# Kernel tuning notes

Hardware: AMD Instinct MI355X
Metric: run time of the kernel (lower is better)

## Reference

```python
import jax, jax.numpy as jnp
import numpy as np
from jax.ops import segment_sum

N_NODES = 100000
N_EDGES = 1600000
N_GRAPHS = 128
HIDDEN = 128
N_CLASSES = 10


def setup_inputs() -> dict:
    key = jax.random.key(0)
    ks = jax.random.split(key, 8)
    src = jax.random.randint(ks[0], (N_EDGES,), 0, N_NODES, dtype=jnp.int32)
    dst = jax.random.randint(ks[1], (N_EDGES,), 0, N_NODES, dtype=jnp.int32)
    graph_ids = jnp.sort(jax.random.randint(ks[2], (N_NODES,), 0, N_GRAPHS, dtype=jnp.int32))
    W1 = jax.random.normal(ks[3], (1, HIDDEN), dtype=jnp.float32)
    b1 = jnp.zeros((HIDDEN,), jnp.float32)
    W2 = jax.random.normal(ks[4], (HIDDEN, HIDDEN), dtype=jnp.float32) * 0.05
    b2 = jnp.zeros((HIDDEN,), jnp.float32)
    Wc = jax.random.normal(ks[5], (HIDDEN, N_CLASSES), dtype=jnp.float32) * 0.05
    bc = jnp.zeros((N_CLASSES,), jnp.float32)
    return {"src": src, "dst": dst, "graph_ids": graph_ids,
            "W1": W1, "b1": b1, "W2": W2, "b2": b2, "Wc": Wc, "bc": bc}


def _graph_conv(h, src, dst, norm_src, norm_dst, W, b, n_nodes):
    # DGL GraphConv, norm='both': D_out^{-1/2} gather -> scatter-sum -> W -> D_in^{-1/2} -> +b
    hs = h * norm_src[:, None]
    agg = segment_sum(hs[src], dst, num_segments=n_nodes)  # [N, F_in]
    return agg @ W * norm_dst[:, None] + b


def reference(src, dst, graph_ids, W1, b1, W2, b2, Wc, bc):
    n_nodes = graph_ids.shape[0]
    ones_e = jnp.ones(src.shape[0], jnp.float32)
    indeg = segment_sum(ones_e, dst, num_segments=n_nodes)
    outdeg = segment_sum(ones_e, src, num_segments=n_nodes)
    norm_src = jnp.clip(outdeg, 1.0, None) ** -0.5
    norm_dst = jnp.clip(indeg, 1.0, None) ** -0.5

    h = indeg[:, None]  # node feature = in-degree, [N, 1]
    h = jax.nn.relu(_graph_conv(h, src, dst, norm_src, norm_dst, W1, b1, n_nodes))
    h = jax.nn.relu(_graph_conv(h, src, dst, norm_src, norm_dst, W2, b2, n_nodes))

    # dgl.mean_nodes: per-graph mean pooling
    sums = segment_sum(h, graph_ids, num_segments=N_GRAPHS)          # [G, H]
    cnts = segment_sum(jnp.ones(n_nodes, jnp.float32), graph_ids, num_segments=N_GRAPHS)
    hg = sums / jnp.clip(cnts, 1.0, None)[:, None]
    return hg @ Wc + bc  # [G, n_classes]
```

## Files before the change

kernel.cpp:

```cpp
#include <hip/hip_runtime.h>

#define N_NODES   100000
#define N_EDGES   1600000
#define N_GRAPHS  128
#define HIDDEN    128
#define N_CLASSES 10

#define BSH   9
#define BSZ   512
#define NBUCK 196
#define CAP   16384
#define PCH   4096
#define PTH   512
#define PIT   (PCH / PTH)

typedef unsigned int   uint;
typedef unsigned short ushort;
typedef unsigned char  uchar;

__global__ __launch_bounds__(PTH)
void k_part(const int* __restrict__ src, const int* __restrict__ dst,
            unsigned* __restrict__ bcur1, unsigned* __restrict__ bcur2,
            unsigned* __restrict__ tmp1, ushort* __restrict__ tmp2, int nE) {
    __shared__ unsigned hist[256], scanT[256], lcur[256], base[256];
    __shared__ unsigned stag4[PCH];
    __shared__ uchar    stagB[PCH];
    int t = threadIdx.x;
    int e0 = blockIdx.x * PCH;
    int e1 = min(e0 + PCH, nE);
    int cntE = e1 - e0;

    int sv[PIT], dv[PIT];
    if (t < 256) hist[t] = 0;
    __syncthreads();
    #pragma unroll
    for (int m = 0; m < PIT; ++m) {
        int e = e0 + t + m * PTH;
        if (e < e1) {
            sv[m] = src[e]; dv[m] = dst[e];
            atomicAdd(&hist[dv[m] >> BSH], 1u);
        }
    }
    __syncthreads();
    unsigned v = (t < 256) ? hist[t] : 0u;
    if (t < 256) scanT[t] = v;
    __syncthreads();
    for (int off = 1; off < 256; off <<= 1) {
        unsigned add = (t < 256 && t >= off) ? scanT[t - off] : 0u;
        __syncthreads();
        if (t < 256) scanT[t] += add;
        __syncthreads();
    }
    if (t < 256) {
        unsigned excl = scanT[t] - v;
        lcur[t] = excl;
        if (v > 0) { unsigned g = atomicAdd(&bcur1[t], v); base[t] = (unsigned)t * CAP + g - excl; }
    }
    __syncthreads();
    #pragma unroll
    for (int m = 0; m < PIT; ++m) {
        int e = e0 + t + m * PTH;
        if (e < e1) {
            int d = dv[m], s = sv[m];
            int b = d >> BSH;
            unsigned p = atomicAdd(&lcur[b], 1u);
            stag4[p] = ((unsigned)(d & (BSZ - 1)) << 17) | (unsigned)s;
            stagB[p] = (uchar)b;
        }
    }
    __syncthreads();
    for (int i = t; i < cntE; i += PTH) {
        unsigned b = stagB[i];
        unsigned a = base[b] + (unsigned)i;
        if (a < (b + 1u) * CAP) tmp1[a] = stag4[i];
    }
    __syncthreads();

    if (t < 256) hist[t] = 0;
    __syncthreads();
    #pragma unroll
    for (int m = 0; m < PIT; ++m) {
        int e = e0 + t + m * PTH;
        if (e < e1) atomicAdd(&hist[sv[m] >> BSH], 1u);
    }
    __syncthreads();
    v = (t < 256) ? hist[t] : 0u;
    if (t < 256) scanT[t] = v;
    __syncthreads();
    for (int off = 1; off < 256; off <<= 1) {
        unsigned add = (t < 256 && t >= off) ? scanT[t - off] : 0u;
        __syncthreads();
        if (t < 256) scanT[t] += add;
        __syncthreads();
    }
    if (t < 256) {
        unsigned excl = scanT[t] - v;
        lcur[t] = excl;
        if (v > 0) { unsigned g = atomicAdd(&bcur2[t], v); base[t] = (unsigned)t * CAP + g - excl; }
    }
    __syncthreads();
    #pragma unroll
    for (int m = 0; m < PIT; ++m) {
        int e = e0 + t + m * PTH;
        if (e < e1) {
            int s = sv[m];
            unsigned p = atomicAdd(&lcur[s >> BSH], 1u);
            stag4[p] = (unsigned)s;
        }
    }
    __syncthreads();
    for (int i = t; i < cntE; i += PTH) {
        unsigned s = stag4[i];
        unsigned b = s >> BSH;
        unsigned a = base[b] + (unsigned)i;
        if (a < (b + 1u) * CAP) tmp2[a] = (ushort)(s & (BSZ - 1));
    }
}

__global__ __launch_bounds__(1024)
void k_ind_csr(const unsigned* __restrict__ bcur1, const unsigned* __restrict__ tmp1,
               const unsigned* __restrict__ bcur2, const ushort* __restrict__ tmp2,
               unsigned* __restrict__ rsind, float* __restrict__ ns,
               float* __restrict__ hs0, int* __restrict__ csr) {
    __shared__ unsigned cin[BSZ], cout[BSZ], pref[BSZ], lcur[BSZ];
    int b = blockIdx.x, t = threadIdx.x;
    if (t < BSZ) { cin[t] = 0; cout[t] = 0; }
    __syncthreads();
    unsigned f1 = min(bcur1[b], (unsigned)CAP);
    const unsigned* tp1 = tmp1 + (size_t)b * CAP;
    for (unsigned i = t; i < f1; i += 1024) atomicAdd(&cin[tp1[i] >> 17], 1u);
    unsigned f2 = min(bcur2[b], (unsigned)CAP);
    const ushort* tp2 = tmp2 + (size_t)b * CAP;
    for (unsigned i = t; i < f2; i += 1024) atomicAdd(&cout[tp2[i]], 1u);
    __syncthreads();
    unsigned v = (t < BSZ) ? cin[t] : 0u;
    if (t < BSZ) pref[t] = v;
    __syncthreads();
    for (int off = 1; off < BSZ; off <<= 1) {
        unsigned add = (t < BSZ && t >= off) ? pref[t - off] : 0u;
        __syncthreads();
        if (t < BSZ) pref[t] += add;
        __syncthreads();
    }
    if (t < BSZ) {
        unsigned excl = pref[t] - v;
        lcur[t] = excl;
        int n = b * BSZ + t;
        if (n < N_NODES) {
            unsigned co = cout[t];
            float nsv = rsqrtf(fmaxf((float)co, 1.0f));
            ns[n]    = nsv;
            hs0[n]   = (float)v * nsv;
            rsind[n] = (((unsigned)b * CAP + excl) << 10) | min(v, 1023u);
        }
    }
    __syncthreads();
    int* cb = csr + (size_t)b * CAP;
    for (unsigned i = t; i < f1; i += 1024) {
        unsigned e = tp1[i];
        unsigned pos = atomicAdd(&lcur[e >> 17], 1u);
        cb[pos] = (int)(e & 0x1FFFFu);
    }
}

__global__ __launch_bounds__(256)
void k_conv1_info(const unsigned* __restrict__ rsind, const int* __restrict__ csr,
                  const float* __restrict__ hs0, const float* __restrict__ ns,
                  const float* __restrict__ W1, const float* __restrict__ b1,
                  const float* __restrict__ W2,
                  float* __restrict__ U, float* __restrict__ V,
                  float4* __restrict__ info, int nN) {
    __shared__ float stu[128];
    __shared__ float sts[128];
    int t = threadIdx.x;
    if (t < 128) {
        float w = W1[t], bb = b1[t];
        stu[t] = (w != 0.0f) ? (-bb / w) : 1e30f;
    }
    __syncthreads();
    if (blockIdx.x < 129) {
        if (t < 128) sts[t] = stu[t];
        __syncthreads();
        for (int k = 2; k <= 128; k <<= 1) {
            for (int j = k >> 1; j > 0; j >>= 1) {
                if (t < 128) {
                    int ixj = t ^ j;
                    if (ixj > t) {
                        float a = sts[t], bb = sts[ixj];
                        bool up = ((t & k) == 0);
                        if (up ? (a > bb) : (a < bb)) { sts[t] = bb; sts[ixj] = a; }
                    }
                }
                __syncthreads();
            }
        }
        if (t < 128) {
            int sg = blockIdx.x;
            float a_rep;
            if (sg == 0)        a_rep = sts[0]   - 1.0f;
            else if (sg == 128) a_rep = sts[127] + 1.0f;
            else                a_rep = 0.5f * (sts[sg - 1] + sts[sg]);
            float u = 0.0f, vv = 0.0f;
            #pragma unroll 8
            for (int j = 0; j < 128; ++j) {
                float w  = W1[j], bb = b1[j];
                float w2 = W2[j * HIDDEN + t];
                bool on  = (a_rep * w + bb > 0.0f);
                u  += on ? w  * w2 : 0.0f;
                vv += on ? bb * w2 : 0.0f;
            }
            U[sg * HIDDEN + t] = u;
            V[sg * HIDDEN + t] = vv;
        }
    }
    int node = blockIdx.x * 128 + (t >> 1);
    if (node >= nN) return;
    int j  = t & 1;
    unsigned rix = rsind[node];
    int r0 = (int)(rix >> 10);
    int c  = (int)(rix & 1023u);
    float a = 0.0f;
    #pragma unroll 4
    for (int k = j; k < c; k += 2) a += hs0[csr[r0 + k]];
    a += __shfl_xor(a, 1);
    float nd = rsqrtf(fmaxf((float)c, 1.0f));
    float av = a * nd;
    int sgp = 0;
    #pragma unroll
    for (int q = 0; q < 64; ++q) sgp += (stu[j * 64 + q] < av) ? 1 : 0;
    sgp += __shfl_xor(sgp, 1);
    if (j == 0) {
        float nsv = ns[node];
        info[node] = make_float4(nsv * av, nsv, __int_as_float(sgp), nd);
    }
}

__global__ __launch_bounds__(256)
void k_conv2_pool(const unsigned* __restrict__ rsind, const int* __restrict__ csr,
                  const float4* __restrict__ info,
                  const float* __restrict__ U, const float* __restrict__ V,
                  const int* __restrict__ graph_ids, const float* __restrict__ b2,
                  float* __restrict__ pool, float* __restrict__ cnt, int nN) {
    __shared__ float sA[64], sB[64], sND[64];
    __shared__ int   sSg[64], sGr[64], sR[64], sC[64];
    __shared__ float sRes[64][HIDDEN];
    int blockBase = blockIdx.x * 64;
    int t = threadIdx.x;
    int node = blockBase + (t >> 2);
    int j = t & 3;

    float A = 0.0f, B = 0.0f;
    int mn = 255, mx = 0;
    int r0 = 0, c = 0;
    if (node < nN) {
        unsigned rix = rsind[node];
        r0 = (int)(rix >> 10); c = (int)(rix & 1023u);
        #pragma unroll 4
        for (int k = j; k < c; k += 4) {
            float4 nf = info[csr[r0 + k]];
            int sg = __float_as_int(nf.z);
            A += nf.x; B += nf.y;
            mn = min(mn, sg); mx = max(mx, sg);
        }
    }
    A += __shfl_xor(A, 1); A += __shfl_xor(A, 2);
    B += __shfl_xor(B, 1); B += __shfl_xor(B, 2);
    mn = min(mn, __shfl_xor(mn, 1)); mn = min(mn, __shfl_xor(mn, 2));
    mx = max(mx, __shfl_xor(mx, 1)); mx = max(mx, __shfl_xor(mx, 2));
    if (node < nN && j == 0) {
        int i = t >> 2;
        sA[i] = A; sB[i] = B;
        sSg[i] = (mn << 8) | mx;
        sR[i] = r0; sC[i] = c;
        sND[i] = info[node].w;
        sGr[i] = graph_ids[node];
    }
    __syncthreads();

    int w = t >> 6, lane = t & 63;
    float bb0 = b2[lane], bb1 = b2[64 + lane];
    for (int i = w * 16; i < w * 16 + 16; ++i) {
        int n = blockBase + i;
        if (n >= nN) break;
        int pk = sSg[i], smn = pk >> 8, smx = pk & 255;
        float acc0, acc1;
        if (smn >= smx) {
            int sg = min(smn, 128);
            float Av = sA[i], Bv = sB[i];
            const float* Ur = U + sg * HIDDEN;
            const float* Vr = V + sg * HIDDEN;
            acc0 = Av * Ur[lane]      + Bv * Vr[lane];
            acc1 = Av * Ur[64 + lane] + Bv * Vr[64 + lane];
        } else {
            acc0 = 0.0f; acc1 = 0.0f;
            int rr = sR[i], cc = sC[i];
            for (int k = 0; k < cc; ++k) {
                float4 nf = info[csr[rr + k]];
                int sg = __float_as_int(nf.z);
                const float* Ur = U + sg * HIDDEN;
                const float* Vr = V + sg * HIDDEN;
                acc0 += nf.x * Ur[lane]      + nf.y * Vr[lane];
                acc1 += nf.x * Ur[64 + lane] + nf.y * Vr[64 + lane];
            }
        }
        float nd = sND[i];
        sRes[i][lane]      = fmaxf(nd * acc0 + bb0, 0.0f);
        sRes[i][64 + lane] = fmaxf(nd * acc1 + bb1, 0.0f);
    }
    __syncthreads();

    if (t >= 64) return;
    int lane0 = t;
    int gcur = -1;
    float racc0 = 0.0f, racc1 = 0.0f, cl = 0.0f;
    for (int i = 0; i < 64; ++i) {
        int n = blockBase + i;
        if (n >= nN) break;
        float r0v = sRes[i][lane0];
        float r1v = sRes[i][64 + lane0];
        int g = sGr[i];
        if (g != gcur) {
            if (gcur >= 0) {
                atomicAdd(&pool[gcur * HIDDEN + lane0],      racc0);
                atomicAdd(&pool[gcur * HIDDEN + 64 + lane0], racc1);
                if (lane0 == 0) atomicAdd(&cnt[gcur], cl);
            }
            gcur = g; racc0 = 0.0f; racc1 = 0.0f; cl = 0.0f;
        }
        racc0 += r0v; racc1 += r1v; cl += 1.0f;
    }
    if (gcur >= 0) {
        atomicAdd(&pool[gcur * HIDDEN + lane0],      racc0);
        atomicAdd(&pool[gcur * HIDDEN + 64 + lane0], racc1);
        if (lane0 == 0) atomicAdd(&cnt[gcur], cl);
    }
}

__global__ void k_final(const float* __restrict__ pool, const float* __restrict__ cnt,
                        const float* __restrict__ Wc, const float* __restrict__ bc,
                        float* __restrict__ out) {
    int t = blockIdx.x * blockDim.x + threadIdx.x;
    if (t >= N_GRAPHS * N_CLASSES) return;
    int g = t / N_CLASSES, c = t % N_CLASSES;
    float inv = 1.0f / fmaxf(cnt[g], 1.0f);
    float acc = bc[c];
    for (int j = 0; j < HIDDEN; ++j)
        acc += pool[g * HIDDEN + j] * inv * Wc[j * N_CLASSES + c];
    out[t] = acc;
}

extern "C" void kernel_launch(void* const* d_in, const int* in_sizes, int n_in,
                              void* d_out, int out_size, void* d_ws, size_t ws_size,
                              hipStream_t stream) {
    const int*   src       = (const int*)d_in[0];
    const int*   dst       = (const int*)d_in[1];
    const int*   graph_ids = (const int*)d_in[2];
    const float* W1        = (const float*)d_in[3];
    const float* b1        = (const float*)d_in[4];
    const float* W2        = (const float*)d_in[5];
    const float* b2        = (const float*)d_in[6];
    const float* Wc        = (const float*)d_in[7];
    const float* bc        = (const float*)d_in[8];
    float* out = (float*)d_out;

    char* ws = (char*)d_ws;
    size_t off = 0;
    auto alloc = [&](size_t elems) { void* p = ws + off; off += elems * 4; return p; };

    unsigned* bcur1 = (unsigned*)alloc(256);
    unsigned* bcur2 = (unsigned*)alloc(256);
    float*    pool  = (float*)   alloc(N_GRAPHS * HIDDEN);
    float*    cnt   = (float*)   alloc(N_GRAPHS);
    size_t zero_bytes = off;
    float4*   info  = (float4*)  alloc((size_t)N_NODES * 4);
    unsigned* tmp1  = (unsigned*)alloc((size_t)NBUCK * CAP);
    ushort*   tmp2  = (ushort*)  alloc((size_t)NBUCK * CAP / 2);
    int*      csr   = (int*)     alloc((size_t)NBUCK * CAP);
    unsigned* rsind = (unsigned*)alloc(N_NODES);
    float*    nsA   = (float*)   alloc(N_NODES);
    float*    hs0   = (float*)   alloc(N_NODES);
    float*    U     = (float*)   alloc(129 * HIDDEN);
    float*    V     = (float*)   alloc(129 * HIDDEN);

    hipMemsetAsync(d_ws, 0, zero_bytes, stream);

    int pblocks  = (N_EDGES + PCH - 1) / PCH;
    int c1blocks = (N_NODES + 127) / 128;
    int c2blocks = (N_NODES + 63) / 64;
    k_part      <<<pblocks, PTH, 0, stream>>>(src, dst, bcur1, bcur2, tmp1, tmp2, N_EDGES);
    k_ind_csr   <<<NBUCK, 1024, 0, stream>>>(bcur1, tmp1, bcur2, tmp2, rsind, nsA, hs0, csr);
    k_conv1_info<<<c1blocks, 256, 0, stream>>>(rsind, csr, hs0, nsA, W1, b1, W2, U, V, info, N_NODES);
    k_conv2_pool<<<c2blocks, 256, 0, stream>>>(rsind, csr, info, U, V, graph_ids, b2, pool, cnt, N_NODES);
    k_final     <<<(N_GRAPHS * N_CLASSES + 255) / 256, 256, 0, stream>>>(pool, cnt, Wc, bc, out);
}
```

Before: 169.1 us.

## Replace bucketed CSR partitioning with global atomic degree count, scan and fill

The two-stage bucket partition (LDS histograms, staging buffers, per-bucket CSR build) is replaced by three simpler passes. k_deg counts in- and out-degree with global atomics, k_scan does a block-wise prefix scan using an atomic block base, and k_fill places edges into the CSR with atomic cursors. k_fill also accumulates the first-layer aggregation with float atomics, so conv1 no longer needs a separate CSR gather. The aim is to cut the partition overhead and one full edge traversal. The cost is millions of random global atomics, a nondeterministic CSR order and a nondeterministic float summation order.

```diff
diff --git a/kernel.cpp b/kernel.cpp
--- a/kernel.cpp
+++ b/kernel.cpp
@@ -6,170 +6,77 @@
 #define HIDDEN    128
 #define N_CLASSES 10
 
-#define BSH   9
-#define BSZ   512
-#define NBUCK 196
-#define CAP   16384
-#define PCH   4096
-#define PTH   512
-#define PIT   (PCH / PTH)
-
 typedef unsigned int   uint;
 typedef unsigned short ushort;
-typedef unsigned char  uchar;
-
-__global__ __launch_bounds__(PTH)
-void k_part(const int* __restrict__ src, const int* __restrict__ dst,
-            unsigned* __restrict__ bcur1, unsigned* __restrict__ bcur2,
-            unsigned* __restrict__ tmp1, ushort* __restrict__ tmp2, int nE) {
-    __shared__ unsigned hist[256], scanT[256], lcur[256], base[256];
-    __shared__ unsigned stag4[PCH];
-    __shared__ uchar    stagB[PCH];
+
+__global__ __launch_bounds__(256)
+void k_deg(const int4* __restrict__ src4, const int4* __restrict__ dst4,
+           uint* __restrict__ indeg, uint* __restrict__ outdeg, int nE4) {
+    int i = blockIdx.x * 256 + threadIdx.x;
+    if (i >= nE4) return;
+    int4 s = src4[i], d = dst4[i];
+    atomicAdd(&outdeg[s.x], 1u); atomicAdd(&outdeg[s.y], 1u);
+    atomicAdd(&outdeg[s.z], 1u); atomicAdd(&outdeg[s.w], 1u);
+    atomicAdd(&indeg[d.x], 1u);  atomicAdd(&indeg[d.y], 1u);
+    atomicAdd(&indeg[d.z], 1u);  atomicAdd(&indeg[d.w], 1u);
+}
+
+__global__ __launch_bounds__(1024)
+void k_scan(const uint* __restrict__ indeg, const uint* __restrict__ outdeg,
+            uint* __restrict__ etotal, uint* __restrict__ cur,
+            uint* __restrict__ rsind, float* __restrict__ ns,
+            float* __restrict__ hs0, int nN) {
+    __shared__ uint sc[1024];
+    __shared__ uint sbase;
     int t = threadIdx.x;
-    int e0 = blockIdx.x * PCH;
-    int e1 = min(e0 + PCH, nE);
-    int cntE = e1 - e0;
-
-    int sv[PIT], dv[PIT];
-    if (t < 256) hist[t] = 0;
-    __syncthreads();
-    #pragma unroll
-    for (int m = 0; m < PIT; ++m) {
-        int e = e0 + t + m * PTH;
-        if (e < e1) {
-            sv[m] = src[e]; dv[m] = dst[e];
-            atomicAdd(&hist[dv[m] >> BSH], 1u);
-        }
-    }
-    __syncthreads();
-    unsigned v = (t < 256) ? hist[t] : 0u;
-    if (t < 256) scanT[t] = v;
-    __syncthreads();
-    for (int off = 1; off < 256; off <<= 1) {
-        unsigned add = (t < 256 && t >= off) ? scanT[t - off] : 0u;
+    int n = blockIdx.x * 1024 + t;
+    uint v = (n < nN) ? indeg[n] : 0u;
+    sc[t] = v;
+    __syncthreads();
+    for (int off = 1; off < 1024; off <<= 1) {
+        uint add = (t >= off) ? sc[t - off] : 0u;
         __syncthreads();
-        if (t < 256) scanT[t] += add;
+        sc[t] += add;
         __syncthreads();
     }
-    if (t < 256) {
-        unsigned excl = scanT[t] - v;
-        lcur[t] = excl;
-        if (v > 0) { unsigned g = atomicAdd(&bcur1[t], v); base[t] = (unsigned)t * CAP + g - excl; }
-    }
-    __syncthreads();
-    #pragma unroll
-    for (int m = 0; m < PIT; ++m) {
-        int e = e0 + t + m * PTH;
-        if (e < e1) {
-            int d = dv[m], s = sv[m];
-            int b = d >> BSH;
-            unsigned p = atomicAdd(&lcur[b], 1u);
-            stag4[p] = ((unsigned)(d & (BSZ - 1)) << 17) | (unsigned)s;
-            stagB[p] = (uchar)b;
-        }
-    }
-    __syncthreads();
-    for (int i = t; i < cntE; i += PTH) {
-        unsigned b = stagB[i];
-        unsigned a = base[b] + (unsigned)i;
-        if (a < (b + 1u) * CAP) tmp1[a] = stag4[i];
-    }
-    __syncthreads();
-
-    if (t < 256) hist[t] = 0;
-    __syncthreads();
-    #pragma unroll
-    for (int m = 0; m < PIT; ++m) {
-        int e = e0 + t + m * PTH;
-        if (e < e1) atomicAdd(&hist[sv[m] >> BSH], 1u);
-    }
-    __syncthreads();
-    v = (t < 256) ? hist[t] : 0u;
-    if (t < 256) scanT[t] = v;
-    __syncthreads();
-    for (int off = 1; off < 256; off <<= 1) {
-        unsigned add = (t < 256 && t >= off) ? scanT[t - off] : 0u;
-        __syncthreads();
-        if (t < 256) scanT[t] += add;
-        __syncthreads();
-    }
-    if (t < 256) {
-        unsigned excl = scanT[t] - v;
-        lcur[t] = excl;
-        if (v > 0) { unsigned g = atomicAdd(&bcur2[t], v); base[t] = (unsigned)t * CAP + g - excl; }
-    }
-    __syncthreads();
-    #pragma unroll
-    for (int m = 0; m < PIT; ++m) {
-        int e = e0 + t + m * PTH;
-        if (e < e1) {
-            int s = sv[m];
-            unsigned p = atomicAdd(&lcur[s >> BSH], 1u);
-            stag4[p] = (unsigned)s;
-        }
-    }
-    __syncthreads();
-    for (int i = t; i < cntE; i += PTH) {
-        unsigned s = stag4[i];
-        unsigned b = s >> BSH;
-        unsigned a = base[b] + (unsigned)i;
-        if (a < (b + 1u) * CAP) tmp2[a] = (ushort)(s & (BSZ - 1));
-    }
-}
-
-__global__ __launch_bounds__(1024)
-void k_ind_csr(const unsigned* __restrict__ bcur1, const unsigned* __restrict__ tmp1,
-               const unsigned* __restrict__ bcur2, const ushort* __restrict__ tmp2,
-               unsigned* __restrict__ rsind, float* __restrict__ ns,
-               float* __restrict__ hs0, int* __restrict__ csr) {
-    __shared__ unsigned cin[BSZ], cout[BSZ], pref[BSZ], lcur[BSZ];
-    int b = blockIdx.x, t = threadIdx.x;
-    if (t < BSZ) { cin[t] = 0; cout[t] = 0; }
-    __syncthreads();
-    unsigned f1 = min(bcur1[b], (unsigned)CAP);
-    const unsigned* tp1 = tmp1 + (size_t)b * CAP;
-    for (unsigned i = t; i < f1; i += 1024) atomicAdd(&cin[tp1[i] >> 17], 1u);
-    unsigned f2 = min(bcur2[b], (unsigned)CAP);
-    const ushort* tp2 = tmp2 + (size_t)b * CAP;
-    for (unsigned i = t; i < f2; i += 1024) atomicAdd(&cout[tp2[i]], 1u);
-    __syncthreads();
-    unsigned v = (t < BSZ) ? cin[t] : 0u;
-    if (t < BSZ) pref[t] = v;
-    __syncthreads();
-    for (int off = 1; off < BSZ; off <<= 1) {
-        unsigned add = (t < BSZ && t >= off) ? pref[t - off] : 0u;
-        __syncthreads();
-        if (t < BSZ) pref[t] += add;
-        __syncthreads();
-    }
-    if (t < BSZ) {
-        unsigned excl = pref[t] - v;
-        lcur[t] = excl;
-        int n = b * BSZ + t;
-        if (n < N_NODES) {
-            unsigned co = cout[t];
-            float nsv = rsqrtf(fmaxf((float)co, 1.0f));
-            ns[n]    = nsv;
-            hs0[n]   = (float)v * nsv;
-            rsind[n] = (((unsigned)b * CAP + excl) << 10) | min(v, 1023u);
-        }
-    }
-    __syncthreads();
-    int* cb = csr + (size_t)b * CAP;
-    for (unsigned i = t; i < f1; i += 1024) {
-        unsigned e = tp1[i];
-        unsigned pos = atomicAdd(&lcur[e >> 17], 1u);
-        cb[pos] = (int)(e & 0x1FFFFu);
+    if (t == 1023) sbase = atomicAdd(etotal, sc[1023]);
+    __syncthreads();
+    if (n < nN) {
+        uint incl = sc[t];
+        uint row  = sbase + incl - v;
+        uint od   = outdeg[n];
+        float nsv = rsqrtf(fmaxf((float)od, 1.0f));
+        ns[n]    = nsv;
+        hs0[n]   = (float)v * nsv;
+        cur[n]   = row;
+        rsind[n] = (row << 10) | min(v, 1023u);
     }
 }
 
 __global__ __launch_bounds__(256)
-void k_conv1_info(const unsigned* __restrict__ rsind, const int* __restrict__ csr,
-                  const float* __restrict__ hs0, const float* __restrict__ ns,
-                  const float* __restrict__ W1, const float* __restrict__ b1,
-                  const float* __restrict__ W2,
-                  float* __restrict__ U, float* __restrict__ V,
-                  float4* __restrict__ info, int nN) {
+void k_fill(const int4* __restrict__ src4, const int4* __restrict__ dst4,
+            const float* __restrict__ hs0, uint* __restrict__ cur,
+            int* __restrict__ csr, float* __restrict__ agg1, int nE4) {
+    int i = blockIdx.x * 256 + threadIdx.x;
+    if (i >= nE4) return;
+    int4 s = src4[i], d = dst4[i];
+    float h0 = hs0[s.x], h1 = hs0[s.y], h2 = hs0[s.z], h3 = hs0[s.w];
+    uint p0 = atomicAdd(&cur[d.x], 1u);
+    uint p1 = atomicAdd(&cur[d.y], 1u);
+    uint p2 = atomicAdd(&cur[d.z], 1u);
+    uint p3 = atomicAdd(&cur[d.w], 1u);
+    csr[p0] = s.x; csr[p1] = s.y; csr[p2] = s.z; csr[p3] = s.w;
+    atomicAdd(&agg1[d.x], h0); atomicAdd(&agg1[d.y], h1);
+    atomicAdd(&agg1[d.z], h2); atomicAdd(&agg1[d.w], h3);
+}
+
+__global__ __launch_bounds__(256)
+void k_info(const uint* __restrict__ indeg, const float* __restrict__ agg1,
+            const float* __restrict__ ns,
+            const float* __restrict__ W1, const float* __restrict__ b1,
+            const float* __restrict__ W2,
+            float* __restrict__ U, float* __restrict__ V,
+            float4* __restrict__ info, int nN) {
     __shared__ float stu[128];
     __shared__ float sts[128];
     int t = threadIdx.x;
@@ -213,30 +120,20 @@
             V[sg * HIDDEN + t] = vv;
         }
     }
-    int node = blockIdx.x * 128 + (t >> 1);
+    int node = blockIdx.x * 256 + t;
     if (node >= nN) return;
-    int j  = t & 1;
-    unsigned rix = rsind[node];
-    int r0 = (int)(rix >> 10);
-    int c  = (int)(rix & 1023u);
-    float a = 0.0f;
-    #pragma unroll 4
-    for (int k = j; k < c; k += 2) a += hs0[csr[r0 + k]];
-    a += __shfl_xor(a, 1);
+    uint c   = indeg[node];
     float nd = rsqrtf(fmaxf((float)c, 1.0f));
-    float av = a * nd;
+    float av = agg1[node] * nd;
     int sgp = 0;
-    #pragma unroll
-    for (int q = 0; q < 64; ++q) sgp += (stu[j * 64 + q] < av) ? 1 : 0;
-    sgp += __shfl_xor(sgp, 1);
-    if (j == 0) {
-        float nsv = ns[node];
-        info[node] = make_float4(nsv * av, nsv, __int_as_float(sgp), nd);
-    }
+    #pragma unroll 16
+    for (int q = 0; q < 128; ++q) sgp += (stu[q] < av) ? 1 : 0;
+    float nsv = ns[node];
+    info[node] = make_float4(nsv * av, nsv, __int_as_float(sgp), nd);
 }
 
 __global__ __launch_bounds__(256)
-void k_conv2_pool(const unsigned* __restrict__ rsind, const int* __restrict__ csr,
+void k_conv2_pool(const uint* __restrict__ rsind, const int* __restrict__ csr,
                   const float4* __restrict__ info,
                   const float* __restrict__ U, const float* __restrict__ V,
                   const int* __restrict__ graph_ids, const float* __restrict__ b2,
@@ -253,7 +150,7 @@
     int mn = 255, mx = 0;
     int r0 = 0, c = 0;
     if (node < nN) {
-        unsigned rix = rsind[node];
+        uint rix = rsind[node];
         r0 = (int)(rix >> 10); c = (int)(rix & 1023u);
         #pragma unroll 4
         for (int k = j; k < c; k += 4) {
@@ -367,29 +264,39 @@
     size_t off = 0;
     auto alloc = [&](size_t elems) { void* p = ws + off; off += elems * 4; return p; };
 
-    unsigned* bcur1 = (unsigned*)alloc(256);
-    unsigned* bcur2 = (unsigned*)alloc(256);
-    float*    pool  = (float*)   alloc(N_GRAPHS * HIDDEN);
-    float*    cnt   = (float*)   alloc(N_GRAPHS);
+    uint*  indeg  = (uint*) alloc(N_NODES);
+    uint*  outdeg = (uint*) alloc(N_NODES);
+    float* agg1   = (float*)alloc(N_NODES);
+    float* pool   = (float*)alloc(N_GRAPHS * HIDDEN);
+    float* cnt    = (float*)alloc(N_GRAPHS);
+    uint*  etotal = (uint*) alloc(4);
     size_t zero_bytes = off;
-    float4*   info  = (float4*)  alloc((size_t)N_NODES * 4);
-    unsigned* tmp1  = (unsigned*)alloc((size_t)NBUCK * CAP);
-    ushort*   tmp2  = (ushort*)  alloc((size_t)NBUCK * CAP / 2);
-    int*      csr   = (int*)     alloc((size_t)NBUCK * CAP);
-    unsigned* rsind = (unsigned*)alloc(N_NODES);
-    float*    nsA   = (float*)   alloc(N_NODES);
-    float*    hs0   = (float*)   alloc(N_NODES);
-    float*    U     = (float*)   alloc(129 * HIDDEN);
-    float*    V     = (float*)   alloc(129 * HIDDEN);
+    uint*   cur   = (uint*)  alloc(N_NODES);
+    uint*   rsind = (uint*)  alloc(N_NODES);
+    float*  nsA   = (float*) alloc(N_NODES);
+    float*  hs0   = (float*) alloc(N_NODES);
+    float4* info  = (float4*)alloc((size_t)N_NODES * 4);
+    int*    csr   = (int*)   alloc((size_t)N_EDGES);
+    float*  U     = (float*) alloc(129 * HIDDEN);
+    float*  V     = (float*) alloc(129 * HIDDEN);
 
     hipMemsetAsync(d_ws, 0, zero_bytes, stream);
 
-    int pblocks  = (N_EDGES + PCH - 1) / PCH;
-    int c1blocks = (N_NODES + 127) / 128;
+    int nE4      = N_EDGES / 4;
+    int eblocks  = (nE4 + 255) / 256;
+    int sblocks  = (N_NODES + 1023) / 1024;
+    int iblocks  = (N_NODES + 255) / 256;
     int c2blocks = (N_NODES + 63) / 64;
-    k_part      <<<pblocks, PTH, 0, stream>>>(src, dst, bcur1, bcur2, tmp1, tmp2, N_EDGES);
-    k_ind_csr   <<<NBUCK, 1024, 0, stream>>>(bcur1, tmp1, bcur2, tmp2, rsind, nsA, hs0, csr);
-    k_conv1_info<<<c1blocks, 256, 0, stream>>>(rsind, csr, hs0, nsA, W1, b1, W2, U, V, info, N_NODES);
-    k_conv2_pool<<<c2blocks, 256, 0, stream>>>(rsind, csr, info, U, V, graph_ids, b2, pool, cnt, N_NODES);
+
+    k_deg       <<<eblocks, 256, 0, stream>>>((const int4*)src, (const int4*)dst,
+                                              indeg, outdeg, nE4);
+    k_scan      <<<sblocks, 1024, 0, stream>>>(indeg, outdeg, etotal, cur,
+                                               rsind, nsA, hs0, N_NODES);
+    k_fill      <<<eblocks, 256, 0, stream>>>((const int4*)src, (const int4*)dst,
+                                              hs0, cur, csr, agg1, nE4);
+    k_info      <<<iblocks, 256, 0, stream>>>(indeg, agg1, nsA, W1, b1, W2,
+                                              U, V, info, N_NODES);
+    k_conv2_pool<<<c2blocks, 256, 0, stream>>>(rsind, csr, info, U, V,
+                                               graph_ids, b2, pool, cnt, N_NODES);
     k_final     <<<(N_GRAPHS * N_CLASSES + 255) / 256, 256, 0, stream>>>(pool, cnt, Wc, bc, out);
 }
```

New measurement: 412.4 us. 144% more time.

## Drop CSR build; aggregate per-bucket edges via shared-memory atomics

Applied to the files above, without the earlier changes.

Removes the per-bucket prefix scan and CSR scatter. Both convolution stages now work directly on the bucketed edge list, with one block per 512-node bucket accumulating into shared memory through atomics. The mixed-segment fallback rescans the whole bucket edge list for each node that needs it. Only 196 blocks are launched, so the GPU is underutilised, and the fallback path can be very expensive.

```diff
diff --git a/kernel.cpp b/kernel.cpp
--- a/kernel.cpp
+++ b/kernel.cpp
@@ -118,11 +118,10 @@
 }
 
 __global__ __launch_bounds__(1024)
-void k_ind_csr(const unsigned* __restrict__ bcur1, const unsigned* __restrict__ tmp1,
-               const unsigned* __restrict__ bcur2, const ushort* __restrict__ tmp2,
-               unsigned* __restrict__ rsind, float* __restrict__ ns,
-               float* __restrict__ hs0, int* __restrict__ csr) {
-    __shared__ unsigned cin[BSZ], cout[BSZ], pref[BSZ], lcur[BSZ];
+void k_cnt(const unsigned* __restrict__ bcur1, const unsigned* __restrict__ tmp1,
+           const unsigned* __restrict__ bcur2, const ushort* __restrict__ tmp2,
+           float* __restrict__ ns, float* __restrict__ hs0, float* __restrict__ ndv) {
+    __shared__ unsigned cin[BSZ], cout[BSZ];
     int b = blockIdx.x, t = threadIdx.x;
     if (t < BSZ) { cin[t] = 0; cout[t] = 0; }
     __syncthreads();
@@ -133,52 +132,37 @@
     const ushort* tp2 = tmp2 + (size_t)b * CAP;
     for (unsigned i = t; i < f2; i += 1024) atomicAdd(&cout[tp2[i]], 1u);
     __syncthreads();
-    unsigned v = (t < BSZ) ? cin[t] : 0u;
-    if (t < BSZ) pref[t] = v;
-    __syncthreads();
-    for (int off = 1; off < BSZ; off <<= 1) {
-        unsigned add = (t < BSZ && t >= off) ? pref[t - off] : 0u;
-        __syncthreads();
-        if (t < BSZ) pref[t] += add;
-        __syncthreads();
-    }
     if (t < BSZ) {
-        unsigned excl = pref[t] - v;
-        lcur[t] = excl;
         int n = b * BSZ + t;
         if (n < N_NODES) {
-            unsigned co = cout[t];
-            float nsv = rsqrtf(fmaxf((float)co, 1.0f));
-            ns[n]    = nsv;
-            hs0[n]   = (float)v * nsv;
-            rsind[n] = (((unsigned)b * CAP + excl) << 10) | min(v, 1023u);
-        }
-    }
-    __syncthreads();
-    int* cb = csr + (size_t)b * CAP;
-    for (unsigned i = t; i < f1; i += 1024) {
-        unsigned e = tp1[i];
-        unsigned pos = atomicAdd(&lcur[e >> 17], 1u);
-        cb[pos] = (int)(e & 0x1FFFFu);
-    }
-}
-
-__global__ __launch_bounds__(256)
-void k_conv1_info(const unsigned* __restrict__ rsind, const int* __restrict__ csr,
-                  const float* __restrict__ hs0, const float* __restrict__ ns,
-                  const float* __restrict__ W1, const float* __restrict__ b1,
-                  const float* __restrict__ W2,
-                  float* __restrict__ U, float* __restrict__ V,
-                  float4* __restrict__ info, int nN) {
+            unsigned ci = cin[t];
+            float nsv = rsqrtf(fmaxf((float)cout[t], 1.0f));
+            ns[n]  = nsv;
+            hs0[n] = (float)ci * nsv;
+            ndv[n] = rsqrtf(fmaxf((float)ci, 1.0f));
+        }
+    }
+}
+
+__global__ __launch_bounds__(512)
+void k_info(const unsigned* __restrict__ bcur1, const unsigned* __restrict__ tmp1,
+            const float* __restrict__ hs0, const float* __restrict__ ns,
+            const float* __restrict__ ndv,
+            const float* __restrict__ W1, const float* __restrict__ b1,
+            const float* __restrict__ W2,
+            float* __restrict__ U, float* __restrict__ V,
+            float4* __restrict__ info) {
+    __shared__ float agg[BSZ];
     __shared__ float stu[128];
     __shared__ float sts[128];
-    int t = threadIdx.x;
+    int b = blockIdx.x, t = threadIdx.x;
+    agg[t] = 0.0f;
     if (t < 128) {
         float w = W1[t], bb = b1[t];
         stu[t] = (w != 0.0f) ? (-bb / w) : 1e30f;
     }
     __syncthreads();
-    if (blockIdx.x < 129) {
+    if (b < 129) {
         if (t < 128) sts[t] = stu[t];
         __syncthreads();
         for (int k = 2; k <= 128; k <<= 1) {
@@ -195,7 +179,7 @@
             }
         }
         if (t < 128) {
-            int sg = blockIdx.x;
+            int sg = b;
             float a_rep;
             if (sg == 0)        a_rep = sts[0]   - 1.0f;
             else if (sg == 128) a_rep = sts[127] + 1.0f;
@@ -213,126 +197,88 @@
             V[sg * HIDDEN + t] = vv;
         }
     }
-    int node = blockIdx.x * 128 + (t >> 1);
-    if (node >= nN) return;
-    int j  = t & 1;
-    unsigned rix = rsind[node];
-    int r0 = (int)(rix >> 10);
-    int c  = (int)(rix & 1023u);
-    float a = 0.0f;
-    #pragma unroll 4
-    for (int k = j; k < c; k += 2) a += hs0[csr[r0 + k]];
-    a += __shfl_xor(a, 1);
-    float nd = rsqrtf(fmaxf((float)c, 1.0f));
-    float av = a * nd;
-    int sgp = 0;
-    #pragma unroll
-    for (int q = 0; q < 64; ++q) sgp += (stu[j * 64 + q] < av) ? 1 : 0;
-    sgp += __shfl_xor(sgp, 1);
-    if (j == 0) {
-        float nsv = ns[node];
-        info[node] = make_float4(nsv * av, nsv, __int_as_float(sgp), nd);
-    }
-}
-
-__global__ __launch_bounds__(256)
-void k_conv2_pool(const unsigned* __restrict__ rsind, const int* __restrict__ csr,
-                  const float4* __restrict__ info,
-                  const float* __restrict__ U, const float* __restrict__ V,
-                  const int* __restrict__ graph_ids, const float* __restrict__ b2,
-                  float* __restrict__ pool, float* __restrict__ cnt, int nN) {
-    __shared__ float sA[64], sB[64], sND[64];
-    __shared__ int   sSg[64], sGr[64], sR[64], sC[64];
-    __shared__ float sRes[64][HIDDEN];
-    int blockBase = blockIdx.x * 64;
-    int t = threadIdx.x;
-    int node = blockBase + (t >> 2);
-    int j = t & 3;
-
-    float A = 0.0f, B = 0.0f;
-    int mn = 255, mx = 0;
-    int r0 = 0, c = 0;
-    if (node < nN) {
-        unsigned rix = rsind[node];
-        r0 = (int)(rix >> 10); c = (int)(rix & 1023u);
-        #pragma unroll 4
-        for (int k = j; k < c; k += 4) {
-            float4 nf = info[csr[r0 + k]];
-            int sg = __float_as_int(nf.z);
-            A += nf.x; B += nf.y;
-            mn = min(mn, sg); mx = max(mx, sg);
-        }
-    }
-    A += __shfl_xor(A, 1); A += __shfl_xor(A, 2);
-    B += __shfl_xor(B, 1); B += __shfl_xor(B, 2);
-    mn = min(mn, __shfl_xor(mn, 1)); mn = min(mn, __shfl_xor(mn, 2));
-    mx = max(mx, __shfl_xor(mx, 1)); mx = max(mx, __shfl_xor(mx, 2));
-    if (node < nN && j == 0) {
-        int i = t >> 2;
-        sA[i] = A; sB[i] = B;
-        sSg[i] = (mn << 8) | mx;
-        sR[i] = r0; sC[i] = c;
-        sND[i] = info[node].w;
-        sGr[i] = graph_ids[node];
-    }
-    __syncthreads();
-
-    int w = t >> 6, lane = t & 63;
-    float bb0 = b2[lane], bb1 = b2[64 + lane];
-    for (int i = w * 16; i < w * 16 + 16; ++i) {
-        int n = blockBase + i;
-        if (n >= nN) break;
-        int pk = sSg[i], smn = pk >> 8, smx = pk & 255;
-        float acc0, acc1;
-        if (smn >= smx) {
-            int sg = min(smn, 128);
-            float Av = sA[i], Bv = sB[i];
-            const float* Ur = U + sg * HIDDEN;
-            const float* Vr = V + sg * HIDDEN;
-            acc0 = Av * Ur[lane]      + Bv * Vr[lane];
-            acc1 = Av * Ur[64 + lane] + Bv * Vr[64 + lane];
+    unsigned f1 = min(bcur1[b], (unsigned)CAP);
+    const unsigned* tp1 = tmp1 + (size_t)b * CAP;
+    for (unsigned i = t; i < f1; i += 512) {
+        unsigned e = tp1[i];
+        atomicAdd(&agg[e >> 17], hs0[e & 0x1FFFFu]);
+    }
+    __syncthreads();
+    int n = b * BSZ + t;
+    if (n < N_NODES) {
+        float nd = ndv[n];
+        float av = agg[t] * nd;
+        int sgp = 0;
+        #pragma unroll 16
+        for (int q = 0; q < 128; ++q) sgp += (stu[q] < av) ? 1 : 0;
+        float nsv = ns[n];
+        info[n] = make_float4(nsv * av, nsv, __int_as_float(sgp), nd);
+    }
+}
+
+__global__ __launch_bounds__(512)
+void k_conv2(const unsigned* __restrict__ bcur1, const unsigned* __restrict__ tmp1,
+             const float4* __restrict__ info,
+             const float* __restrict__ U, const float* __restrict__ V,
+             const int* __restrict__ graph_ids, const float* __restrict__ b2,
+             float* __restrict__ pool, float* __restrict__ cnt) {
+    __shared__ float aggA[BSZ], aggB[BSZ];
+    __shared__ uint  smn[BSZ], smx[BSZ];
+    int b = blockIdx.x, t = threadIdx.x;
+    aggA[t] = 0.0f; aggB[t] = 0.0f; smn[t] = 255u; smx[t] = 0u;
+    __syncthreads();
+    unsigned f1 = min(bcur1[b], (unsigned)CAP);
+    const unsigned* tp1 = tmp1 + (size_t)b * CAP;
+    for (unsigned i = t; i < f1; i += 512) {
+        unsigned e = tp1[i];
+        unsigned dl = e >> 17;
+        float4 nf = info[e & 0x1FFFFu];
+        atomicAdd(&aggA[dl], nf.x);
+        atomicAdd(&aggB[dl], nf.y);
+        uint sg = (uint)__float_as_int(nf.z);
+        atomicMin(&smn[dl], sg);
+        atomicMax(&smx[dl], sg);
+    }
+    __syncthreads();
+
+    int d = t & 127, q = t >> 7;
+    float bbd = b2[d];
+    int base = b * BSZ;
+    int nmax = min(BSZ, N_NODES - base);
+    int gcur = -1; float racc = 0.0f, cl = 0.0f;
+    for (int i = q; i < nmax; i += 4) {
+        int n = base + i;
+        uint mn = smn[i], mx = smx[i];
+        float acc;
+        if (mn >= mx) {
+            uint sg = min(mn, 128u);
+            acc = aggA[i] * U[sg * HIDDEN + d] + aggB[i] * V[sg * HIDDEN + d];
         } else {
-            acc0 = 0.0f; acc1 = 0.0f;
-            int rr = sR[i], cc = sC[i];
-            for (int k = 0; k < cc; ++k) {
-                float4 nf = info[csr[rr + k]];
-                int sg = __float_as_int(nf.z);
-                const float* Ur = U + sg * HIDDEN;
-                const float* Vr = V + sg * HIDDEN;
-                acc0 += nf.x * Ur[lane]      + nf.y * Vr[lane];
-                acc1 += nf.x * Ur[64 + lane] + nf.y * Vr[64 + lane];
+            acc = 0.0f;
+            for (unsigned k = 0; k < f1; ++k) {
+                unsigned e = tp1[k];
+                if ((e >> 17) == (unsigned)i) {
+                    float4 nf = info[e & 0x1FFFFu];
+                    uint sg = (uint)__float_as_int(nf.z);
+                    acc += nf.x * U[sg * HIDDEN + d] + nf.y * V[sg * HIDDEN + d];
+                }
             }
         }
-        float nd = sND[i];
-        sRes[i][lane]      = fmaxf(nd * acc0 + bb0, 0.0f);
-        sRes[i][64 + lane] = fmaxf(nd * acc1 + bb1, 0.0f);
-    }
-    __syncthreads();
-
-    if (t >= 64) return;
-    int lane0 = t;
-    int gcur = -1;
-    float racc0 = 0.0f, racc1 = 0.0f, cl = 0.0f;
-    for (int i = 0; i < 64; ++i) {
-        int n = blockBase + i;
-        if (n >= nN) break;
-        float r0v = sRes[i][lane0];
-        float r1v = sRes[i][64 + lane0];
-        int g = sGr[i];
+        float nd = info[n].w;
+        float row = fmaxf(nd * acc + bbd, 0.0f);
+        int g = graph_ids[n];
         if (g != gcur) {
             if (gcur >= 0) {
-                atomicAdd(&pool[gcur * HIDDEN + lane0],      racc0);
-                atomicAdd(&pool[gcur * HIDDEN + 64 + lane0], racc1);
-                if (lane0 == 0) atomicAdd(&cnt[gcur], cl);
+                atomicAdd(&pool[gcur * HIDDEN + d], racc);
+                if (d == 0) atomicAdd(&cnt[gcur], cl);
             }
-            gcur = g; racc0 = 0.0f; racc1 = 0.0f; cl = 0.0f;
-        }
-        racc0 += r0v; racc1 += r1v; cl += 1.0f;
+            gcur = g; racc = 0.0f; cl = 0.0f;
+        }
+        racc += row; cl += 1.0f;
     }
     if (gcur >= 0) {
-        atomicAdd(&pool[gcur * HIDDEN + lane0],      racc0);
-        atomicAdd(&pool[gcur * HIDDEN + 64 + lane0], racc1);
-        if (lane0 == 0) atomicAdd(&cnt[gcur], cl);
+        atomicAdd(&pool[gcur * HIDDEN + d], racc);
+        if (d == 0) atomicAdd(&cnt[gcur], cl);
     }
 }
 
@@ -375,21 +321,18 @@
     float4*   info  = (float4*)  alloc((size_t)N_NODES * 4);
     unsigned* tmp1  = (unsigned*)alloc((size_t)NBUCK * CAP);
     ushort*   tmp2  = (ushort*)  alloc((size_t)NBUCK * CAP / 2);
-    int*      csr   = (int*)     alloc((size_t)NBUCK * CAP);
-    unsigned* rsind = (unsigned*)alloc(N_NODES);
     float*    nsA   = (float*)   alloc(N_NODES);
     float*    hs0   = (float*)   alloc(N_NODES);
+    float*    ndv   = (float*)   alloc(N_NODES);
     float*    U     = (float*)   alloc(129 * HIDDEN);
     float*    V     = (float*)   alloc(129 * HIDDEN);
 
     hipMemsetAsync(d_ws, 0, zero_bytes, stream);
 
-    int pblocks  = (N_EDGES + PCH - 1) / PCH;
-    int c1blocks = (N_NODES + 127) / 128;
-    int c2blocks = (N_NODES + 63) / 64;
-    k_part      <<<pblocks, PTH, 0, stream>>>(src, dst, bcur1, bcur2, tmp1, tmp2, N_EDGES);
-    k_ind_csr   <<<NBUCK, 1024, 0, stream>>>(bcur1, tmp1, bcur2, tmp2, rsind, nsA, hs0, csr);
-    k_conv1_info<<<c1blocks, 256, 0, stream>>>(rsind, csr, hs0, nsA, W1, b1, W2, U, V, info, N_NODES);
-    k_conv2_pool<<<c2blocks, 256, 0, stream>>>(rsind, csr, info, U, V, graph_ids, b2, pool, cnt, N_NODES);
-    k_final     <<<(N_GRAPHS * N_CLASSES + 255) / 256, 256, 0, stream>>>(pool, cnt, Wc, bc, out);
-}
+    int pblocks = (N_EDGES + PCH - 1) / PCH;
+    k_part <<<pblocks, PTH, 0, stream>>>(src, dst, bcur1, bcur2, tmp1, tmp2, N_EDGES);
+    k_cnt  <<<NBUCK, 1024, 0, stream>>>(bcur1, tmp1, bcur2, tmp2, nsA, hs0, ndv);
+    k_info <<<NBUCK, 512, 0, stream>>>(bcur1, tmp1, hs0, nsA, ndv, W1, b1, W2, U, V, info);
+    k_conv2<<<NBUCK, 512, 0, stream>>>(bcur1, tmp1, info, U, V, graph_ids, b2, pool, cnt);
+    k_final<<<(N_GRAPHS * N_CLASSES + 255) / 256, 256, 0, stream>>>(pool, cnt, Wc, bc, out);
+}
```

Measured after the change: 190.3 us. 12.6% more time.

## Replace out-degree partition pass with global atomics and shrink buckets

Applied to the files above, without the earlier changes.

Drops the second src-based partition (tmp2 staging, scans and scatter) in the partition kernel and instead counts out-degree directly with global atomicAdd per edge into a zeroed array. Buckets shrink from 512 to 256 nodes, giving 391 buckets with 8192 capacity each, and the shared-memory Hillis-Steele scans become wavefront shuffle scans. The per-bucket CSR kernel now unrolls its counting loop and reads out-degree from the global array. The change trades a partition pass and its memory traffic for 1.6M scattered global atomics, a larger memset, and more, smaller CSR blocks.

```diff
diff --git a/kernel.cpp b/kernel.cpp
--- a/kernel.cpp
+++ b/kernel.cpp
@@ -6,32 +6,52 @@
 #define HIDDEN    128
 #define N_CLASSES 10
 
-#define BSH   9
-#define BSZ   512
-#define NBUCK 196
-#define CAP   16384
+#define BSH   8
+#define BSZ   256
+#define NBUCK 391
+#define NPAD  (NBUCK * BSZ)
+#define NBIN  512
+#define CAP   8192
 #define PCH   4096
 #define PTH   512
 #define PIT   (PCH / PTH)
 
 typedef unsigned int   uint;
 typedef unsigned short ushort;
-typedef unsigned char  uchar;
+
+__device__ __forceinline__ uint scan_excl_512(uint v, int t, uint* wtmp) {
+    uint lane = (uint)(t & 63);
+    uint incl = v;
+    #pragma unroll
+    for (int off = 1; off < 64; off <<= 1) {
+        uint up = __shfl_up(incl, off, 64);
+        if (lane >= (uint)off) incl += up;
+    }
+    if (lane == 63) wtmp[t >> 6] = incl;
+    __syncthreads();
+    uint wo = 0;
+    int w = t >> 6;
+    #pragma unroll
+    for (int k = 0; k < 7; ++k) wo += (k < w) ? wtmp[k] : 0u;
+    __syncthreads();
+    return incl + wo - v;
+}
 
 __global__ __launch_bounds__(PTH)
 void k_part(const int* __restrict__ src, const int* __restrict__ dst,
-            unsigned* __restrict__ bcur1, unsigned* __restrict__ bcur2,
-            unsigned* __restrict__ tmp1, ushort* __restrict__ tmp2, int nE) {
-    __shared__ unsigned hist[256], scanT[256], lcur[256], base[256];
-    __shared__ unsigned stag4[PCH];
-    __shared__ uchar    stagB[PCH];
+            uint* __restrict__ bcur1, uint* __restrict__ outdeg,
+            uint* __restrict__ tmp1, int nE) {
+    __shared__ uint   hist[NBIN], lcur[NBIN], base[NBIN];
+    __shared__ uint   wtmp[8];
+    __shared__ uint   stag4[PCH];
+    __shared__ ushort stagB[PCH];
     int t = threadIdx.x;
     int e0 = blockIdx.x * PCH;
     int e1 = min(e0 + PCH, nE);
     int cntE = e1 - e0;
 
     int sv[PIT], dv[PIT];
-    if (t < 256) hist[t] = 0;
+    hist[t] = 0;
     __syncthreads();
     #pragma unroll
     for (int m = 0; m < PIT; ++m) {
@@ -39,23 +59,14 @@
         if (e < e1) {
             sv[m] = src[e]; dv[m] = dst[e];
             atomicAdd(&hist[dv[m] >> BSH], 1u);
-        }
-    }
-    __syncthreads();
-    unsigned v = (t < 256) ? hist[t] : 0u;
-    if (t < 256) scanT[t] = v;
-    __syncthreads();
-    for (int off = 1; off < 256; off <<= 1) {
-        unsigned add = (t < 256 && t >= off) ? scanT[t - off] : 0u;
-        __syncthreads();
-        if (t < 256) scanT[t] += add;
-        __syncthreads();
-    }
-    if (t < 256) {
-        unsigned excl = scanT[t] - v;
-        lcur[t] = excl;
-        if (v > 0) { unsigned g = atomicAdd(&bcur1[t], v); base[t] = (unsigned)t * CAP + g - excl; }
-    }
+            atomicAdd(&outdeg[sv[m]], 1u);
+        }
+    }
+    __syncthreads();
+    uint v = hist[t];
+    uint excl = scan_excl_512(v, t, wtmp);
+    lcur[t] = excl;
+    if (v > 0) { uint g = atomicAdd(&bcur1[t], v); base[t] = (uint)t * CAP + g - excl; }
     __syncthreads();
     #pragma unroll
     for (int m = 0; m < PIT; ++m) {
@@ -63,108 +74,79 @@
         if (e < e1) {
             int d = dv[m], s = sv[m];
             int b = d >> BSH;
-            unsigned p = atomicAdd(&lcur[b], 1u);
-            stag4[p] = ((unsigned)(d & (BSZ - 1)) << 17) | (unsigned)s;
-            stagB[p] = (uchar)b;
+            uint p = atomicAdd(&lcur[b], 1u);
+            stag4[p] = ((uint)(d & (BSZ - 1)) << 17) | (uint)s;
+            stagB[p] = (ushort)b;
         }
     }
     __syncthreads();
     for (int i = t; i < cntE; i += PTH) {
-        unsigned b = stagB[i];
-        unsigned a = base[b] + (unsigned)i;
+        uint b = stagB[i];
+        uint a = base[b] + (uint)i;
         if (a < (b + 1u) * CAP) tmp1[a] = stag4[i];
     }
-    __syncthreads();
-
-    if (t < 256) hist[t] = 0;
-    __syncthreads();
-    #pragma unroll
-    for (int m = 0; m < PIT; ++m) {
-        int e = e0 + t + m * PTH;
-        if (e < e1) atomicAdd(&hist[sv[m] >> BSH], 1u);
-    }
-    __syncthreads();
-    v = (t < 256) ? hist[t] : 0u;
-    if (t < 256) scanT[t] = v;
-    __syncthreads();
-    for (int off = 1; off < 256; off <<= 1) {
-        unsigned add = (t < 256 && t >= off) ? scanT[t - off] : 0u;
-        __syncthreads();
-        if (t < 256) scanT[t] += add;
-        __syncthreads();
-    }
-    if (t < 256) {
-        unsigned excl = scanT[t] - v;
-        lcur[t] = excl;
-        if (v > 0) { unsigned g = atomicAdd(&bcur2[t], v); base[t] = (unsigned)t * CAP + g - excl; }
-    }
-    __syncthreads();
-    #pragma unroll
-    for (int m = 0; m < PIT; ++m) {
-        int e = e0 + t + m * PTH;
-        if (e < e1) {
-            int s = sv[m];
-            unsigned p = atomicAdd(&lcur[s >> BSH], 1u);
-            stag4[p] = (unsigned)s;
-        }
-    }
-    __syncthreads();
-    for (int i = t; i < cntE; i += PTH) {
-        unsigned s = stag4[i];
-        unsigned b = s >> BSH;
-        unsigned a = base[b] + (unsigned)i;
-        if (a < (b + 1u) * CAP) tmp2[a] = (ushort)(s & (BSZ - 1));
-    }
 }
 
 __global__ __launch_bounds__(1024)
-void k_ind_csr(const unsigned* __restrict__ bcur1, const unsigned* __restrict__ tmp1,
-               const unsigned* __restrict__ bcur2, const ushort* __restrict__ tmp2,
-               unsigned* __restrict__ rsind, float* __restrict__ ns,
+void k_cnt_csr(const uint* __restrict__ bcur1, const uint* __restrict__ tmp1,
+               const uint* __restrict__ outdeg,
+               uint* __restrict__ rsind, float* __restrict__ ns,
                float* __restrict__ hs0, int* __restrict__ csr) {
-    __shared__ unsigned cin[BSZ], cout[BSZ], pref[BSZ], lcur[BSZ];
+    __shared__ uint cin[BSZ], lcur[BSZ];
+    __shared__ uint wtmp[4];
     int b = blockIdx.x, t = threadIdx.x;
-    if (t < BSZ) { cin[t] = 0; cout[t] = 0; }
-    __syncthreads();
-    unsigned f1 = min(bcur1[b], (unsigned)CAP);
-    const unsigned* tp1 = tmp1 + (size_t)b * CAP;
-    for (unsigned i = t; i < f1; i += 1024) atomicAdd(&cin[tp1[i] >> 17], 1u);
-    unsigned f2 = min(bcur2[b], (unsigned)CAP);
-    const ushort* tp2 = tmp2 + (size_t)b * CAP;
-    for (unsigned i = t; i < f2; i += 1024) atomicAdd(&cout[tp2[i]], 1u);
-    __syncthreads();
-    unsigned v = (t < BSZ) ? cin[t] : 0u;
-    if (t < BSZ) pref[t] = v;
-    __syncthreads();
-    for (int off = 1; off < BSZ; off <<= 1) {
-        unsigned add = (t < BSZ && t >= off) ? pref[t - off] : 0u;
-        __syncthreads();
-        if (t < BSZ) pref[t] += add;
-        __syncthreads();
-    }
+    if (t < BSZ) cin[t] = 0;
+    __syncthreads();
+    uint f1 = min(bcur1[b], (uint)CAP);
+    const uint* tp1 = tmp1 + (size_t)b * CAP;
+    uint i = t;
+    for (; i + 3072u < f1; i += 4096u) {
+        uint a0 = tp1[i], a1 = tp1[i + 1024], a2 = tp1[i + 2048], a3 = tp1[i + 3072];
+        atomicAdd(&cin[a0 >> 17], 1u); atomicAdd(&cin[a1 >> 17], 1u);
+        atomicAdd(&cin[a2 >> 17], 1u); atomicAdd(&cin[a3 >> 17], 1u);
+    }
+    for (; i < f1; i += 1024u) atomicAdd(&cin[tp1[i] >> 17], 1u);
+    __syncthreads();
+    uint v = 0, incl = 0;
     if (t < BSZ) {
-        unsigned excl = pref[t] - v;
+        v = cin[t];
+        incl = v;
+        uint lane = (uint)(t & 63);
+        #pragma unroll
+        for (int off = 1; off < 64; off <<= 1) {
+            uint up = __shfl_up(incl, off, 64);
+            if (lane >= (uint)off) incl += up;
+        }
+        if (lane == 63) wtmp[t >> 6] = incl;
+    }
+    __syncthreads();
+    if (t < BSZ) {
+        uint wo = 0;
+        int w = t >> 6;
+        #pragma unroll
+        for (int k = 0; k < 3; ++k) wo += (k < w) ? wtmp[k] : 0u;
+        uint excl = incl + wo - v;
         lcur[t] = excl;
         int n = b * BSZ + t;
         if (n < N_NODES) {
-            unsigned co = cout[t];
+            uint co = outdeg[n];
             float nsv = rsqrtf(fmaxf((float)co, 1.0f));
             ns[n]    = nsv;
             hs0[n]   = (float)v * nsv;
-            rsind[n] = (((unsigned)b * CAP + excl) << 10) | min(v, 1023u);
+            rsind[n] = (((uint)b * CAP + excl) << 10) | min(v, 1023u);
         }
     }
     __syncthreads();
     int* cb = csr + (size_t)b * CAP;
-    for (unsigned i = t; i < f1; i += 1024) {
-        unsigned e = tp1[i];
-        unsigned pos = atomicAdd(&lcur[e >> 17], 1u);
+    for (uint j = t; j < f1; j += 1024u) {
+        uint e = tp1[j];
+        uint pos = atomicAdd(&lcur[e >> 17], 1u);
         cb[pos] = (int)(e & 0x1FFFFu);
     }
 }
 
 __global__ __launch_bounds__(256)
-void k_conv1_info(const unsigned* __restrict__ rsind, const int* __restrict__ csr,
+void k_conv1_info(const uint* __restrict__ rsind, const int* __restrict__ csr,
                   const float* __restrict__ hs0, const float* __restrict__ ns,
                   const float* __restrict__ W1, const float* __restrict__ b1,
                   const float* __restrict__ W2,
@@ -216,7 +198,7 @@
     int node = blockIdx.x * 128 + (t >> 1);
     if (node >= nN) return;
     int j  = t & 1;
-    unsigned rix = rsind[node];
+    uint rix = rsind[node];
     int r0 = (int)(rix >> 10);
     int c  = (int)(rix & 1023u);
     float a = 0.0f;
@@ -236,7 +218,7 @@
 }
 
 __global__ __launch_bounds__(256)
-void k_conv2_pool(const unsigned* __restrict__ rsind, const int* __restrict__ csr,
+void k_conv2_pool(const uint* __restrict__ rsind, const int* __restrict__ csr,
                   const float4* __restrict__ info,
                   const float* __restrict__ U, const float* __restrict__ V,
                   const int* __restrict__ graph_ids, const float* __restrict__ b2,
@@ -253,7 +235,7 @@
     int mn = 255, mx = 0;
     int r0 = 0, c = 0;
     if (node < nN) {
-        unsigned rix = rsind[node];
+        uint rix = rsind[node];
         r0 = (int)(rix >> 10); c = (int)(rix & 1023u);
         #pragma unroll 4
         for (int k = j; k < c; k += 4) {
@@ -367,28 +349,28 @@
     size_t off = 0;
     auto alloc = [&](size_t elems) { void* p = ws + off; off += elems * 4; return p; };
 
-    unsigned* bcur1 = (unsigned*)alloc(256);
-    unsigned* bcur2 = (unsigned*)alloc(256);
-    float*    pool  = (float*)   alloc(N_GRAPHS * HIDDEN);
-    float*    cnt   = (float*)   alloc(N_GRAPHS);
+    uint*  bcur1  = (uint*) alloc(NBIN);
+    uint*  outdeg = (uint*) alloc(NPAD);
+    float* pool   = (float*)alloc(N_GRAPHS * HIDDEN);
+    float* cnt    = (float*)alloc(N_GRAPHS);
     size_t zero_bytes = off;
-    float4*   info  = (float4*)  alloc((size_t)N_NODES * 4);
-    unsigned* tmp1  = (unsigned*)alloc((size_t)NBUCK * CAP);
-    ushort*   tmp2  = (ushort*)  alloc((size_t)NBUCK * CAP / 2);
-    int*      csr   = (int*)     alloc((size_t)NBUCK * CAP);
-    unsigned* rsind = (unsigned*)alloc(N_NODES);
-    float*    nsA   = (float*)   alloc(N_NODES);
-    float*    hs0   = (float*)   alloc(N_NODES);
-    float*    U     = (float*)   alloc(129 * HIDDEN);
-    float*    V     = (float*)   alloc(129 * HIDDEN);
+    float4* info  = (float4*)alloc((size_t)NPAD * 4);
+    uint*   tmp1  = (uint*)  alloc((size_t)NBUCK * CAP);
+    int*    csr   = (int*)   alloc((size_t)NBUCK * CAP);
+    uint*   rsind = (uint*)  alloc(NPAD);
+    float*  nsA   = (float*) alloc(NPAD);
+    float*  hs0   = (float*) alloc(NPAD);
+    float*  U     = (float*) alloc(129 * HIDDEN);
+    float*  V     = (float*) alloc(129 * HIDDEN);
 
     hipMemsetAsync(d_ws, 0, zero_bytes, stream);
 
     int pblocks  = (N_EDGES + PCH - 1) / PCH;
     int c1blocks = (N_NODES + 127) / 128;
     int c2blocks = (N_NODES + 63) / 64;
-    k_part      <<<pblocks, PTH, 0, stream>>>(src, dst, bcur1, bcur2, tmp1, tmp2, N_EDGES);
-    k_ind_csr   <<<NBUCK, 1024, 0, stream>>>(bcur1, tmp1, bcur2, tmp2, rsind, nsA, hs0, csr);
+
+    k_part      <<<pblocks, PTH, 0, stream>>>(src, dst, bcur1, outdeg, tmp1, N_EDGES);
+    k_cnt_csr   <<<NBUCK, 1024, 0, stream>>>(bcur1, tmp1, outdeg, rsind, nsA, hs0, csr);
     k_conv1_info<<<c1blocks, 256, 0, stream>>>(rsind, csr, hs0, nsA, W1, b1, W2, U, V, info, N_NODES);
     k_conv2_pool<<<c2blocks, 256, 0, stream>>>(rsind, csr, info, U, V, graph_ids, b2, pool, cnt, N_NODES);
     k_final     <<<(N_GRAPHS * N_CLASSES + 255) / 256, 256, 0, stream>>>(pool, cnt, Wc, bc, out);
```

After: 215.7 us. 27.6% more time.
